# Performance work log

Measured on AMD Instinct MI355X. Metric: run time of the kernel, lower is better.

Reference implementation:

```python
import jax, jax.numpy as jnp
import numpy as np

B, C_IN, H, W = 4, 1536, 64, 64   # SGI input: cat of three 512-ch encoder maps at 64x64
HID, OUT = 1536, 512
N = H * W


def _grid_edge_index(h, w):
    # 4-connected bidirectional grid, matching SGI.grid_edge_index
    idx = np.arange(h * w).reshape(h, w)
    right = np.stack([idx[:, :-1].ravel(), idx[:, 1:].ravel()])
    down = np.stack([idx[:-1, :].ravel(), idx[1:, :].ravel()])
    ei = np.concatenate([right, down, right[::-1], down[::-1]], axis=1)
    return ei.astype(np.int32)


def setup_inputs() -> dict:
    key = jax.random.key(0)
    ks = jax.random.split(key, 7)
    ei = _grid_edge_index(H, W)
    s = 0.02
    return {
        "x":  jax.random.normal(ks[0], (B, C_IN, H, W), jnp.float32),
        "W1": jax.random.normal(ks[1], (C_IN, HID), jnp.float32) * s,
        "b1": jnp.zeros((HID,), jnp.float32),
        "W2": jax.random.normal(ks[2], (HID, OUT), jnp.float32) * s,
        "b2": jnp.zeros((OUT,), jnp.float32),
        "Wl": jax.random.normal(ks[3], (C_IN, OUT), jnp.float32) * s,
        "bl": jnp.zeros((OUT,), jnp.float32),
        "src": jnp.asarray(ei[0]),
        "dst": jnp.asarray(ei[1]),
    }


def _gcn(h_in, Wt, b, src, dst, inv_sqrt_deg, inv_deg):
    # PyG GCNConv: lin -> symmetric-normalized aggregation (with self loops) -> +bias
    h = h_in @ Wt                                   # [B, N, F]
    norm = inv_sqrt_deg[src] * inv_sqrt_deg[dst]    # [E]
    msgs = h[:, src, :] * norm[None, :, None]       # [B, E, F]
    # self-loop contribution has norm 1/deg_i
    agg = (h * inv_deg[None, :, None]).at[:, dst, :].add(msgs)
    return agg + b


def reference(x, W1, b1, W2, b2, Wl, bl, src, dst):
    Bb, C, Hh, Ww = x.shape
    n = Hh * Ww
    # degree including self loop (graph is symmetric)
    deg = jnp.zeros((n,), x.dtype).at[dst].add(1.0) + 1.0
    inv_sqrt_deg = jax.lax.rsqrt(deg)
    inv_deg = 1.0 / deg

    xt = x.reshape(Bb, C, n).transpose(0, 2, 1)     # [B, N, C]
    identity = xt
    origin = xt @ Wl + bl                           # [B, N, OUT]
    h = jax.nn.relu(_gcn(xt, W1, b1, src, dst, inv_sqrt_deg, inv_deg))
    h = _gcn(h + identity, W2, b2, src, dst, inv_sqrt_deg, inv_deg)
    out = h * origin                                # [B, N, OUT]
    return out.transpose(0, 2, 1).reshape(Bb, out.shape[-1], Hh, Ww)
```

## Files before the change

### kernel.cpp

```cpp
#include <hip/hip_runtime.h>
#include <hip/hip_bf16.h>
#include <stdint.h>


typedef __bf16 bf16;
typedef float f32x4 __attribute__((ext_vector_type(4)));
typedef bf16 bf16x8 __attribute__((ext_vector_type(8)));

#define NB 4
#define NN 4096
#define CIN 1536
#define HIDF 1536
#define OUTF 512

__device__ __forceinline__ void tcvt(const float* __restrict__ in,
                                     bf16* __restrict__ out, int R, int Cc,
                                     int c0, int r0, int t,
                                     float (*tile)[33]) {
  const int tx = t & 31, ty = t >> 5;
#pragma unroll
  for (int i = 0; i < 4; i++)
    tile[ty + i * 8][tx] = in[(long)(r0 + ty + i * 8) * Cc + c0 + tx];
  __syncthreads();
#pragma unroll
  for (int i = 0; i < 4; i++)
    out[(long)(c0 + ty + i * 8) * R + r0 + tx] = (bf16)tile[tx][ty + i * 8];
}

#define XTILES (NB * (NN / 32) * (CIN / 32))
#define W1TILES ((CIN / 32) * (HIDF / 32))
#define W2TILES ((HIDF / 32) * (OUTF / 32))
#define WLTILES ((CIN / 32) * (OUTF / 32))

__global__ __launch_bounds__(256) void prep(
    const float* __restrict__ x, const float* __restrict__ W1,
    const float* __restrict__ W2, const float* __restrict__ Wl,
    bf16* __restrict__ xt, bf16* __restrict__ w1t, bf16* __restrict__ w2t,
    bf16* __restrict__ wlt) {
  __shared__ float tile[32][33];
  const int b = blockIdx.x, t = threadIdx.x;
  if (b < XTILES) {
    const int batch = b / (XTILES / NB), local = b % (XTILES / NB);
    const int cx = local & 127, ry = local >> 7;
    tcvt(x + (long)batch * CIN * NN, xt + (long)batch * NN * CIN, CIN, NN,
         cx * 32, ry * 32, t, tile);
  } else if (b < XTILES + W1TILES) {
    const int local = b - XTILES;
    const int cx = local % 48, ry = local / 48;
    tcvt(W1, w1t, CIN, HIDF, cx * 32, ry * 32, t, tile);
  } else if (b < XTILES + W1TILES + W2TILES) {
    const int local = b - XTILES - W1TILES;
    const int cx = local % 16, ry = local / 16;
    tcvt(W2, w2t, HIDF, OUTF, cx * 32, ry * 32, t, tile);
  } else {
    const int local = b - XTILES - W1TILES - W2TILES;
    const int cx = local % 16, ry = local / 16;
    tcvt(Wl, wlt, CIN, OUTF, cx * 32, ry * 32, t, tile);
  }
}

__device__ __forceinline__ void async_copy16(const void* g, void* l) {
  __builtin_amdgcn_global_load_lds(
      (const __attribute__((address_space(1))) void*)g,
      (__attribute__((address_space(3))) void*)l, 16, 0, 0);
}

struct GemmCtx {
  f32x4 acc[4][4];
  int wave, lane, wm, wn, quad, l15;
};

template <int K>
__device__ __forceinline__ void gemm_kloop(GemmCtx& cx, const bf16* Ab,
                                           const bf16* Bb, bf16* As,
                                           bf16* Bs) {
  const int r = cx.lane >> 3, c8 = cx.lane & 7;
  const int fchunk = c8 ^ r;
  for (int kt = 0; kt < K; kt += 64) {
#pragma unroll
    for (int i = 0; i < 4; i++) {
      const int row = i * 32 + cx.wave * 8;
      async_copy16(Ab + (long)(row + r) * K + kt + fchunk * 8, &As[row * 64]);
      async_copy16(Bb + (long)(row + r) * K + kt + fchunk * 8, &Bs[row * 64]);
    }
    __syncthreads();
#pragma unroll
    for (int kk = 0; kk < 2; kk++) {
      const int q = kk * 4 + cx.quad;
      bf16x8 af[4], bfv[4];
#pragma unroll
      for (int mr = 0; mr < 4; mr++) {
        const int m = cx.wm + mr * 16 + cx.l15;
        af[mr] = *(const bf16x8*)&As[m * 64 + (q ^ (m & 7)) * 8];
      }
#pragma unroll
      for (int nc = 0; nc < 4; nc++) {
        const int n = cx.wn + nc * 16 + cx.l15;
        bfv[nc] = *(const bf16x8*)&Bs[n * 64 + (q ^ (n & 7)) * 8];
      }
#pragma unroll
      for (int mr = 0; mr < 4; mr++)
#pragma unroll
        for (int nc = 0; nc < 4; nc++)
          cx.acc[mr][nc] = __builtin_amdgcn_mfma_f32_16x16x32_bf16(
              af[mr], bfv[nc], cx.acc[mr][nc], 0, 0, 0);
    }
    __syncthreads();
  }
}

__device__ __forceinline__ void gemm_init(GemmCtx& cx, int t) {
  cx.wave = t >> 6;
  cx.lane = t & 63;
  cx.wm = (cx.wave & 1) * 64;
  cx.wn = (cx.wave >> 1) * 64;
  cx.quad = cx.lane >> 4;
  cx.l15 = cx.lane & 15;
#pragma unroll
  for (int i = 0; i < 4; i++)
#pragma unroll
    for (int j = 0; j < 4; j++) cx.acc[i][j] = {0.f, 0.f, 0.f, 0.f};
}

__global__ __launch_bounds__(256) void gemm_dual(
    const bf16* __restrict__ A, const bf16* __restrict__ Bw,
    bf16* __restrict__ G1, float* __restrict__ Orig,
    const float* __restrict__ bl) {
  __shared__ bf16 As[128 * 64];
  __shared__ bf16 Bs[128 * 64];
  GemmCtx cx;
  gemm_init(cx, threadIdx.x);
  const int m0 = blockIdx.x * 128, n0 = blockIdx.y * 128, z = blockIdx.z;
  gemm_kloop<CIN>(cx, A + (long)z * NN * CIN + (long)m0 * CIN,
                  Bw + (long)n0 * CIN, As, Bs);
  if (n0 < HIDF) {
    bf16* Cb = G1 + (long)z * NN * HIDF;
#pragma unroll
    for (int mr = 0; mr < 4; mr++)
#pragma unroll
      for (int nc = 0; nc < 4; nc++) {
        const int gn = n0 + cx.wn + nc * 16 + cx.l15;
#pragma unroll
        for (int j = 0; j < 4; j++) {
          const int gm = m0 + cx.wm + mr * 16 + cx.quad * 4 + j;
          Cb[(long)gm * HIDF + gn] = (bf16)cx.acc[mr][nc][j];
        }
      }
  } else {
    float* Cb = Orig + (long)z * NN * OUTF;
#pragma unroll
    for (int mr = 0; mr < 4; mr++)
#pragma unroll
      for (int nc = 0; nc < 4; nc++) {
        const int gn = (n0 - HIDF) + cx.wn + nc * 16 + cx.l15;
        const float bv = bl[gn];
#pragma unroll
        for (int j = 0; j < 4; j++) {
          const int gm = m0 + cx.wm + mr * 16 + cx.quad * 4 + j;
          Cb[(long)gm * OUTF + gn] = cx.acc[mr][nc][j] + bv;
        }
      }
  }
}

__global__ __launch_bounds__(256) void gemm_f32(
    const bf16* __restrict__ A, const bf16* __restrict__ Bw,
    float* __restrict__ C, int Nf) {
  __shared__ bf16 As[128 * 64];
  __shared__ bf16 Bs[128 * 64];
  GemmCtx cx;
  gemm_init(cx, threadIdx.x);
  const int m0 = blockIdx.x * 128, n0 = blockIdx.y * 128, z = blockIdx.z;
  gemm_kloop<HIDF>(cx, A + (long)z * NN * HIDF + (long)m0 * HIDF,
                   Bw + (long)n0 * HIDF, As, Bs);
  float* Cb = C + (long)z * NN * Nf;
#pragma unroll
  for (int mr = 0; mr < 4; mr++)
#pragma unroll
    for (int nc = 0; nc < 4; nc++) {
      const int gn = n0 + cx.wn + nc * 16 + cx.l15;
#pragma unroll
      for (int j = 0; j < 4; j++) {
        const int gm = m0 + cx.wm + mr * 16 + cx.quad * 4 + j;
        Cb[(long)gm * Nf + gn] = cx.acc[mr][nc][j];
      }
    }
}

__device__ __forceinline__ float degree_of(int n) {
  const int x = n & 63, y = n >> 6;
  return 1.0f + (x > 0) + (x < 63) + (y > 0) + (y < 63);
}

__global__ __launch_bounds__(192) void stencil1(
    const bf16* __restrict__ G1, const float* __restrict__ b1, bf16* xt) {
  const int blk = blockIdx.x;
  const int s = ((blk & 7) << 6) + (blk >> 3);
  const int b = blockIdx.y, t = threadIdx.x;
  float bias[8];
  {
    f32x4 b0 = *(const f32x4*)(b1 + t * 8);
    f32x4 b4 = *(const f32x4*)(b1 + t * 8 + 4);
#pragma unroll
    for (int i = 0; i < 4; i++) { bias[i] = b0[i]; bias[4 + i] = b4[i]; }
  }
#pragma unroll 1
  for (int p = 0; p < 8; p++) {
    const int n = s * 8 + p;
    const int gx = n & 63, gy = n >> 6;
    const float degn = degree_of(n);
    const float wself = 1.0f / degn;
    const long base = ((long)b * NN + n) * (long)HIDF + t * 8;
    float acc[8];
    {
      bf16x8 v = *(const bf16x8*)(G1 + base);
#pragma unroll
      for (int i = 0; i < 8; i++) acc[i] = (float)v[i] * wself;
    }
    if (gx > 0) {
      const float w = rsqrtf(degn * degree_of(n - 1));
      bf16x8 u = *(const bf16x8*)(G1 + base - HIDF);
#pragma unroll
      for (int i = 0; i < 8; i++) acc[i] += (float)u[i] * w;
    }
    if (gx < 63) {
      const float w = rsqrtf(degn * degree_of(n + 1));
      bf16x8 u = *(const bf16x8*)(G1 + base + HIDF);
#pragma unroll
      for (int i = 0; i < 8; i++) acc[i] += (float)u[i] * w;
    }
    if (gy > 0) {
      const float w = rsqrtf(degn * degree_of(n - 64));
      bf16x8 u = *(const bf16x8*)(G1 + base - 64L * HIDF);
#pragma unroll
      for (int i = 0; i < 8; i++) acc[i] += (float)u[i] * w;
    }
    if (gy < 63) {
      const float w = rsqrtf(degn * degree_of(n + 64));
      bf16x8 u = *(const bf16x8*)(G1 + base + 64L * HIDF);
#pragma unroll
      for (int i = 0; i < 8; i++) acc[i] += (float)u[i] * w;
    }
    bf16x8 xv = *(const bf16x8*)(xt + base);
    bf16x8 o;
#pragma unroll
    for (int i = 0; i < 8; i++) {
      float h = acc[i] + bias[i];
      h = h > 0.f ? h : 0.f;
      o[i] = (bf16)(h + (float)xv[i]);
    }
    *(bf16x8*)(xt + base) = o;
  }
}

__global__ __launch_bounds__(256) void stencil2(
    const float* __restrict__ G2, const float* __restrict__ Orig,
    const float* __restrict__ b2, float* __restrict__ out) {
  __shared__ float tile[16][513];
  const int blk = blockIdx.x;
  const int s = ((blk & 7) << 5) + (blk >> 3);
  const int n0 = s * 16, b = blockIdx.y;
  const int t = threadIdx.x;
  const int fq = t & 127, nl = t >> 7;
  const int f = fq * 4;
  const f32x4 bv = *(const f32x4*)(b2 + f);
#pragma unroll
  for (int p = 0; p < 8; p++) {
    const int nLoc = p * 2 + nl;
    const int n = n0 + nLoc;
    const int gx = n & 63, gy = n >> 6;
    const float degn = degree_of(n);
    const float ws = 1.0f / degn;
    const long rb = ((long)b * NN + n) * (long)OUTF + f;
    f32x4 g = *(const f32x4*)(G2 + rb);
    f32x4 a;
#pragma unroll
    for (int i = 0; i < 4; i++) a[i] = g[i] * ws;
    if (gx > 0) {
      const float w = rsqrtf(degn * degree_of(n - 1));
      f32x4 u = *(const f32x4*)(G2 + rb - OUTF);
#pragma unroll
      for (int i = 0; i < 4; i++) a[i] += u[i] * w;
    }
    if (gx < 63) {
      const float w = rsqrtf(degn * degree_of(n + 1));
      f32x4 u = *(const f32x4*)(G2 + rb + OUTF);
#pragma unroll
      for (int i = 0; i < 4; i++) a[i] += u[i] * w;
    }
    if (gy > 0) {
      const float w = rsqrtf(degn * degree_of(n - 64));
      f32x4 u = *(const f32x4*)(G2 + rb - 64L * OUTF);
#pragma unroll
      for (int i = 0; i < 4; i++) a[i] += u[i] * w;
    }
    if (gy < 63) {
      const float w = rsqrtf(degn * degree_of(n + 64));
      f32x4 u = *(const f32x4*)(G2 + rb + 64L * OUTF);
#pragma unroll
      for (int i = 0; i < 4; i++) a[i] += u[i] * w;
    }
    f32x4 og = *(const f32x4*)(Orig + rb);
#pragma unroll
    for (int i = 0; i < 4; i++) tile[nLoc][f + i] = (a[i] + bv[i]) * og[i];
  }
  __syncthreads();
  const int nl2 = t & 15, f0 = t >> 4;
#pragma unroll
  for (int q = 0; q < 32; q++) {
    const int ff = q * 16 + f0;
    out[((long)b * OUTF + ff) * (long)NN + n0 + nl2] = tile[nl2][ff];
  }
}

extern "C" void kernel_launch(void* const* d_in, const int* in_sizes, int n_in,
                              void* d_out, int out_size, void* d_ws,
                              size_t ws_size, hipStream_t stream) {
  const float* x = (const float*)d_in[0];
  const float* W1 = (const float*)d_in[1];
  const float* b1 = (const float*)d_in[2];
  const float* W2 = (const float*)d_in[3];
  const float* b2 = (const float*)d_in[4];
  const float* Wl = (const float*)d_in[5];
  const float* bl = (const float*)d_in[6];
  float* out = (float*)d_out;

  uint8_t* ws = (uint8_t*)d_ws;
  size_t off = 0;
  auto alloc = [&](size_t bytes) -> void* {
    void* p = ws + off;
    off += (bytes + 255) & ~(size_t)255;
    return p;
  };
  bf16* xt = (bf16*)alloc((size_t)NB * NN * CIN * 2);
  bf16* g1 = (bf16*)alloc((size_t)NB * NN * HIDF * 2);
  bf16* wcat = (bf16*)alloc((size_t)(HIDF + OUTF) * CIN * 2);
  bf16* w1t = wcat;
  bf16* wlt = wcat + (size_t)HIDF * CIN;
  bf16* w2t = (bf16*)alloc((size_t)OUTF * HIDF * 2);
  float* g2 = (float*)alloc((size_t)NB * NN * OUTF * 4);
  float* origin = (float*)alloc((size_t)NB * NN * OUTF * 4);

  prep<<<XTILES + W1TILES + W2TILES + WLTILES, 256, 0, stream>>>(
      x, W1, W2, Wl, xt, w1t, w2t, wlt);

  gemm_dual<<<dim3(NN / 128, (HIDF + OUTF) / 128, NB), 256, 0, stream>>>(
      xt, wcat, g1, origin, bl);

  stencil1<<<dim3(512, NB), 192, 0, stream>>>(g1, b1, xt);

  gemm_f32<<<dim3(NN / 128, OUTF / 128, NB), 256, 0, stream>>>(xt, w2t, g2,
                                                               OUTF);

  stencil2<<<dim3(256, NB), 256, 0, stream>>>(g2, origin, b2, out);
}
```

Baseline: 394.3 us.

## Aggregate input before first GEMM and fuse bias/ReLU/residual into its epilogue

Uses the associativity A·(X·W1) = (A·X)·W1 to apply the first graph stencil to the fp32 input inside the prep/transposition kernel. Prep now writes both the transposed input and an aggregated copy. The first GEMM's epilogue then adds the bias, applies ReLU and adds the residual directly, so the stencil1 pass and its re-reading of the bf16 G1 intermediate go away. The dual GEMM is split into separate hidden and origin GEMMs, and dead buffers are aliased to reuse workspace. The cost is an extra full-size bf16 write and neighbour reads in prep, plus scattered residual reads in the GEMM epilogue.

Result: slower. 459.8 us (+16.6%).

```diff
diff --git a/kernel.cpp b/kernel.cpp
--- a/kernel.cpp
+++ b/kernel.cpp
@@ -13,6 +13,11 @@
 #define HIDF 1536
 #define OUTF 512
 
+__device__ __forceinline__ float degree_of(int n) {
+  const int x = n & 63, y = n >> 6;
+  return 1.0f + (x > 0) + (x < 63) + (y > 0) + (y < 63);
+}
+
 __device__ __forceinline__ void tcvt(const float* __restrict__ in,
                                      bf16* __restrict__ out, int R, int Cc,
                                      int c0, int r0, int t,
@@ -35,27 +40,54 @@
 __global__ __launch_bounds__(256) void prep(
     const float* __restrict__ x, const float* __restrict__ W1,
     const float* __restrict__ W2, const float* __restrict__ Wl,
-    bf16* __restrict__ xt, bf16* __restrict__ w1t, bf16* __restrict__ w2t,
-    bf16* __restrict__ wlt) {
-  __shared__ float tile[32][33];
+    bf16* __restrict__ xt, bf16* __restrict__ xa, bf16* __restrict__ w1t,
+    bf16* __restrict__ w2t, bf16* __restrict__ wlt) {
+  __shared__ float t1[32][33];
+  __shared__ float t2[32][33];
   const int b = blockIdx.x, t = threadIdx.x;
   if (b < XTILES) {
     const int batch = b / (XTILES / NB), local = b % (XTILES / NB);
-    const int cx = local & 127, ry = local >> 7;
-    tcvt(x + (long)batch * CIN * NN, xt + (long)batch * NN * CIN, CIN, NN,
-         cx * 32, ry * 32, t, tile);
+    const int ntile = (local & 127) * 32, ctile = (local >> 7) * 32;
+    const float* inb = x + (long)batch * CIN * NN;
+    const int tx = t & 31, ty = t >> 5;
+    const int n = ntile + tx;
+    const int gx = n & 63, gy = n >> 6;
+    const float degn = degree_of(n);
+    const float winv = 1.0f / degn;
+    const float wL = (gx > 0) ? rsqrtf(degn * degree_of(n - 1)) : 0.f;
+    const float wR = (gx < 63) ? rsqrtf(degn * degree_of(n + 1)) : 0.f;
+    const float wU = (gy > 0) ? rsqrtf(degn * degree_of(n - 64)) : 0.f;
+    const float wD = (gy < 63) ? rsqrtf(degn * degree_of(n + 64)) : 0.f;
+#pragma unroll
+    for (int i = 0; i < 4; i++) {
+      const float* row = inb + (long)(ctile + ty + i * 8) * NN;
+      const float v = row[n];
+      float a = v * winv;
+      if (gx > 0) a += row[n - 1] * wL;
+      if (gx < 63) a += row[n + 1] * wR;
+      if (gy > 0) a += row[n - 64] * wU;
+      if (gy < 63) a += row[n + 64] * wD;
+      t1[ty + i * 8][tx] = v;
+      t2[ty + i * 8][tx] = a;
+    }
+    __syncthreads();
+    bf16* xtb = xt + (long)batch * NN * CIN;
+    bf16* xab = xa + (long)batch * NN * CIN;
+#pragma unroll
+    for (int i = 0; i < 4; i++) {
+      const long o = (long)(ntile + ty + i * 8) * CIN + ctile + tx;
+      xtb[o] = (bf16)t1[tx][ty + i * 8];
+      xab[o] = (bf16)t2[tx][ty + i * 8];
+    }
   } else if (b < XTILES + W1TILES) {
     const int local = b - XTILES;
-    const int cx = local % 48, ry = local / 48;
-    tcvt(W1, w1t, CIN, HIDF, cx * 32, ry * 32, t, tile);
+    tcvt(W1, w1t, CIN, HIDF, (local % 48) * 32, (local / 48) * 32, t, t1);
   } else if (b < XTILES + W1TILES + W2TILES) {
     const int local = b - XTILES - W1TILES;
-    const int cx = local % 16, ry = local / 16;
-    tcvt(W2, w2t, HIDF, OUTF, cx * 32, ry * 32, t, tile);
+    tcvt(W2, w2t, HIDF, OUTF, (local % 16) * 32, (local / 16) * 32, t, t1);
   } else {
     const int local = b - XTILES - W1TILES - W2TILES;
-    const int cx = local % 16, ry = local / 16;
-    tcvt(Wl, wlt, CIN, OUTF, cx * 32, ry * 32, t, tile);
+    tcvt(Wl, wlt, CIN, OUTF, (local % 16) * 32, (local / 16) * 32, t, t1);
   }
 }
 
@@ -69,6 +101,19 @@
   f32x4 acc[4][4];
   int wave, lane, wm, wn, quad, l15;
 };
+
+__device__ __forceinline__ void gemm_init(GemmCtx& cx, int t) {
+  cx.wave = t >> 6;
+  cx.lane = t & 63;
+  cx.wm = (cx.wave & 1) * 64;
+  cx.wn = (cx.wave >> 1) * 64;
+  cx.quad = cx.lane >> 4;
+  cx.l15 = cx.lane & 15;
+#pragma unroll
+  for (int i = 0; i < 4; i++)
+#pragma unroll
+    for (int j = 0; j < 4; j++) cx.acc[i][j] = {0.f, 0.f, 0.f, 0.f};
+}
 
 template <int K>
 __device__ __forceinline__ void gemm_kloop(GemmCtx& cx, const bf16* Ab,
@@ -109,23 +154,39 @@
   }
 }
 
-__device__ __forceinline__ void gemm_init(GemmCtx& cx, int t) {
-  cx.wave = t >> 6;
-  cx.lane = t & 63;
-  cx.wm = (cx.wave & 1) * 64;
-  cx.wn = (cx.wave >> 1) * 64;
-  cx.quad = cx.lane >> 4;
-  cx.l15 = cx.lane & 15;
-#pragma unroll
-  for (int i = 0; i < 4; i++)
-#pragma unroll
-    for (int j = 0; j < 4; j++) cx.acc[i][j] = {0.f, 0.f, 0.f, 0.f};
-}
-
-__global__ __launch_bounds__(256) void gemm_dual(
+__global__ __launch_bounds__(256) void gemm_h(
+    const bf16* __restrict__ xa, const bf16* __restrict__ w1t,
+    const bf16* __restrict__ xt, bf16* __restrict__ h,
+    const float* __restrict__ b1) {
+  __shared__ bf16 As[128 * 64];
+  __shared__ bf16 Bs[128 * 64];
+  GemmCtx cx;
+  gemm_init(cx, threadIdx.x);
+  const int m0 = blockIdx.x * 128, n0 = blockIdx.y * 128, z = blockIdx.z;
+  gemm_kloop<CIN>(cx, xa + (long)z * NN * CIN + (long)m0 * CIN,
+                  w1t + (long)n0 * CIN, As, Bs);
+  const bf16* Xb = xt + (long)z * NN * HIDF;
+  bf16* Cb = h + (long)z * NN * HIDF;
+#pragma unroll
+  for (int mr = 0; mr < 4; mr++)
+#pragma unroll
+    for (int nc = 0; nc < 4; nc++) {
+      const int gn = n0 + cx.wn + nc * 16 + cx.l15;
+      const float bv = b1[gn];
+#pragma unroll
+      for (int j = 0; j < 4; j++) {
+        const int gm = m0 + cx.wm + mr * 16 + cx.quad * 4 + j;
+        float v = cx.acc[mr][nc][j] + bv;
+        v = v > 0.f ? v : 0.f;
+        Cb[(long)gm * HIDF + gn] = (bf16)(v + (float)Xb[(long)gm * HIDF + gn]);
+      }
+    }
+}
+
+template <bool ADD_BIAS>
+__global__ __launch_bounds__(256) void gemm_f32(
     const bf16* __restrict__ A, const bf16* __restrict__ Bw,
-    bf16* __restrict__ G1, float* __restrict__ Orig,
-    const float* __restrict__ bl) {
+    float* __restrict__ C, const float* __restrict__ bias) {
   __shared__ bf16 As[128 * 64];
   __shared__ bf16 Bs[128 * 64];
   GemmCtx cx;
@@ -133,124 +194,20 @@
   const int m0 = blockIdx.x * 128, n0 = blockIdx.y * 128, z = blockIdx.z;
   gemm_kloop<CIN>(cx, A + (long)z * NN * CIN + (long)m0 * CIN,
                   Bw + (long)n0 * CIN, As, Bs);
-  if (n0 < HIDF) {
-    bf16* Cb = G1 + (long)z * NN * HIDF;
-#pragma unroll
-    for (int mr = 0; mr < 4; mr++)
-#pragma unroll
-      for (int nc = 0; nc < 4; nc++) {
-        const int gn = n0 + cx.wn + nc * 16 + cx.l15;
-#pragma unroll
-        for (int j = 0; j < 4; j++) {
-          const int gm = m0 + cx.wm + mr * 16 + cx.quad * 4 + j;
-          Cb[(long)gm * HIDF + gn] = (bf16)cx.acc[mr][nc][j];
-        }
-      }
-  } else {
-    float* Cb = Orig + (long)z * NN * OUTF;
-#pragma unroll
-    for (int mr = 0; mr < 4; mr++)
-#pragma unroll
-      for (int nc = 0; nc < 4; nc++) {
-        const int gn = (n0 - HIDF) + cx.wn + nc * 16 + cx.l15;
-        const float bv = bl[gn];
-#pragma unroll
-        for (int j = 0; j < 4; j++) {
-          const int gm = m0 + cx.wm + mr * 16 + cx.quad * 4 + j;
-          Cb[(long)gm * OUTF + gn] = cx.acc[mr][nc][j] + bv;
-        }
-      }
-  }
-}
-
-__global__ __launch_bounds__(256) void gemm_f32(
-    const bf16* __restrict__ A, const bf16* __restrict__ Bw,
-    float* __restrict__ C, int Nf) {
-  __shared__ bf16 As[128 * 64];
-  __shared__ bf16 Bs[128 * 64];
-  GemmCtx cx;
-  gemm_init(cx, threadIdx.x);
-  const int m0 = blockIdx.x * 128, n0 = blockIdx.y * 128, z = blockIdx.z;
-  gemm_kloop<HIDF>(cx, A + (long)z * NN * HIDF + (long)m0 * HIDF,
-                   Bw + (long)n0 * HIDF, As, Bs);
-  float* Cb = C + (long)z * NN * Nf;
+  float* Cb = C + (long)z * NN * OUTF;
 #pragma unroll
   for (int mr = 0; mr < 4; mr++)
 #pragma unroll
     for (int nc = 0; nc < 4; nc++) {
       const int gn = n0 + cx.wn + nc * 16 + cx.l15;
+      float bv = 0.f;
+      if (ADD_BIAS) bv = bias[gn];
 #pragma unroll
       for (int j = 0; j < 4; j++) {
         const int gm = m0 + cx.wm + mr * 16 + cx.quad * 4 + j;
-        Cb[(long)gm * Nf + gn] = cx.acc[mr][nc][j];
+        Cb[(long)gm * OUTF + gn] = cx.acc[mr][nc][j] + bv;
       }
     }
-}
-
-__device__ __forceinline__ float degree_of(int n) {
-  const int x = n & 63, y = n >> 6;
-  return 1.0f + (x > 0) + (x < 63) + (y > 0) + (y < 63);
-}
-
-__global__ __launch_bounds__(192) void stencil1(
-    const bf16* __restrict__ G1, const float* __restrict__ b1, bf16* xt) {
-  const int blk = blockIdx.x;
-  const int s = ((blk & 7) << 6) + (blk >> 3);
-  const int b = blockIdx.y, t = threadIdx.x;
-  float bias[8];
-  {
-    f32x4 b0 = *(const f32x4*)(b1 + t * 8);
-    f32x4 b4 = *(const f32x4*)(b1 + t * 8 + 4);
-#pragma unroll
-    for (int i = 0; i < 4; i++) { bias[i] = b0[i]; bias[4 + i] = b4[i]; }
-  }
-#pragma unroll 1
-  for (int p = 0; p < 8; p++) {
-    const int n = s * 8 + p;
-    const int gx = n & 63, gy = n >> 6;
-    const float degn = degree_of(n);
-    const float wself = 1.0f / degn;
-    const long base = ((long)b * NN + n) * (long)HIDF + t * 8;
-    float acc[8];
-    {
-      bf16x8 v = *(const bf16x8*)(G1 + base);
-#pragma unroll
-      for (int i = 0; i < 8; i++) acc[i] = (float)v[i] * wself;
-    }
-    if (gx > 0) {
-      const float w = rsqrtf(degn * degree_of(n - 1));
-      bf16x8 u = *(const bf16x8*)(G1 + base - HIDF);
-#pragma unroll
-      for (int i = 0; i < 8; i++) acc[i] += (float)u[i] * w;
-    }
-    if (gx < 63) {
-      const float w = rsqrtf(degn * degree_of(n + 1));
-      bf16x8 u = *(const bf16x8*)(G1 + base + HIDF);
-#pragma unroll
-      for (int i = 0; i < 8; i++) acc[i] += (float)u[i] * w;
-    }
-    if (gy > 0) {
-      const float w = rsqrtf(degn * degree_of(n - 64));
-      bf16x8 u = *(const bf16x8*)(G1 + base - 64L * HIDF);
-#pragma unroll
-      for (int i = 0; i < 8; i++) acc[i] += (float)u[i] * w;
-    }
-    if (gy < 63) {
-      const float w = rsqrtf(degn * degree_of(n + 64));
-      bf16x8 u = *(const bf16x8*)(G1 + base + 64L * HIDF);
-#pragma unroll
-      for (int i = 0; i < 8; i++) acc[i] += (float)u[i] * w;
-    }
-    bf16x8 xv = *(const bf16x8*)(xt + base);
-    bf16x8 o;
-#pragma unroll
-    for (int i = 0; i < 8; i++) {
-      float h = acc[i] + bias[i];
-      h = h > 0.f ? h : 0.f;
-      o[i] = (bf16)(h + (float)xv[i]);
-    }
-    *(bf16x8*)(xt + base) = o;
-  }
 }
 
 __global__ __launch_bounds__(256) void stencil2(
@@ -333,24 +290,22 @@
     return p;
   };
   bf16* xt = (bf16*)alloc((size_t)NB * NN * CIN * 2);
-  bf16* g1 = (bf16*)alloc((size_t)NB * NN * HIDF * 2);
-  bf16* wcat = (bf16*)alloc((size_t)(HIDF + OUTF) * CIN * 2);
-  bf16* w1t = wcat;
-  bf16* wlt = wcat + (size_t)HIDF * CIN;
+  bf16* xa = (bf16*)alloc((size_t)NB * NN * CIN * 2);
+  bf16* hb = (bf16*)alloc((size_t)NB * NN * HIDF * 2);
+  bf16* w1t = (bf16*)alloc((size_t)HIDF * CIN * 2);
   bf16* w2t = (bf16*)alloc((size_t)OUTF * HIDF * 2);
-  float* g2 = (float*)alloc((size_t)NB * NN * OUTF * 4);
-  float* origin = (float*)alloc((size_t)NB * NN * OUTF * 4);
+  bf16* wlt = (bf16*)alloc((size_t)OUTF * CIN * 2);
+  float* origin = (float*)xa;
+  float* g2 = (float*)xt;
 
   prep<<<XTILES + W1TILES + W2TILES + WLTILES, 256, 0, stream>>>(
-      x, W1, W2, Wl, xt, w1t, w2t, wlt);
-
-  gemm_dual<<<dim3(NN / 128, (HIDF + OUTF) / 128, NB), 256, 0, stream>>>(
-      xt, wcat, g1, origin, bl);
-
-  stencil1<<<dim3(512, NB), 192, 0, stream>>>(g1, b1, xt);
-
-  gemm_f32<<<dim3(NN / 128, OUTF / 128, NB), 256, 0, stream>>>(xt, w2t, g2,
-                                                               OUTF);
-
+      x, W1, W2, Wl, xt, xa, w1t, w2t, wlt);
+
+  gemm_h<<<dim3(NN / 128, HIDF / 128, NB), 256, 0, stream>>>(xa, w1t, xt, hb,
+                                                             b1);
+  gemm_f32<true><<<dim3(NN / 128, OUTF / 128, NB), 256, 0, stream>>>(
+      xt, wlt, origin, bl);
+  gemm_f32<false><<<dim3(NN / 128, OUTF / 128, NB), 256, 0, stream>>>(
+      hb, w2t, g2, nullptr);
   stencil2<<<dim3(256, NB), 256, 0, stream>>>(g2, origin, b2, out);
 }
```
